# Performance work log

Measured on AMD Instinct MI355X. Metric: run time of the kernel, lower is better.

The kernel has to match this reference:

```python
import jax, jax.numpy as jnp
import numpy as np

B, T, C = 8, 1024, 1024
H, D = 16, 64  # num_heads, head_size

def setup_inputs() -> dict:
    key = jax.random.key(0)
    ks = jax.random.split(key, 6)
    s = C ** -0.5
    return {
        "x": jax.random.normal(ks[0], (B, T, C), dtype=jnp.float32),
        "Wq": jax.random.normal(ks[1], (H, C, D), dtype=jnp.float32) * s,
        "Wk": jax.random.normal(ks[2], (H, C, D), dtype=jnp.float32) * s,
        "Wv": jax.random.normal(ks[3], (H, C, D), dtype=jnp.float32) * s,
        "Wproj": jax.random.normal(ks[4], (H * D, C), dtype=jnp.float32) * ((H * D) ** -0.5),
        "bproj": jnp.zeros((C,), dtype=jnp.float32),
    }

def reference(x, Wq, Wk, Wv, Wproj, bproj):
    # per-head QKV projections, batched over heads via einsum (same math as looped heads)
    q = jnp.einsum('btc,hcd->bhtd', x, Wq)
    k = jnp.einsum('btc,hcd->bhtd', x, Wk)
    v = jnp.einsum('btc,hcd->bhtd', x, Wv)
    scale = D ** -0.5  # k.shape[-1]**-0.5 in original head
    scores = jnp.einsum('bhtd,bhsd->bhts', q, k) * scale  # [B,H,T,T]
    Tn = x.shape[1]
    causal = jnp.tril(jnp.ones((Tn, Tn), dtype=bool))
    scores = jnp.where(causal, scores, jnp.float32(-jnp.inf))
    att = jax.nn.softmax(scores, axis=-1)
    out = jnp.einsum('bhts,bhsd->bhtd', att, v)          # [B,H,T,D]
    out = out.transpose(0, 2, 1, 3).reshape(x.shape[0], Tn, H * D)  # concat heads
    return out @ Wproj + bproj  # dropout is identity at p=0.0
```

## Files before the change

### kernel.cpp

```cpp
#include <hip/hip_runtime.h>
#include <hip/hip_bf16.h>

#define B_ 8
#define T_ 1024
#define C_ 1024
#define H_ 16
#define D_ 64
#define QKVLD 3072

typedef short v8s __attribute__((ext_vector_type(8)));
typedef float v4f __attribute__((ext_vector_type(4)));
typedef float v16f __attribute__((ext_vector_type(16)));

__device__ __forceinline__ unsigned short f2b(float f) {
    unsigned int u = __builtin_bit_cast(unsigned int, f);
    unsigned int lsb = (u >> 16) & 1u;
    u += 0x7fffu + lsb;
    return (unsigned short)(u >> 16);
}

__device__ __forceinline__ float fexp2(float x) {
#if __has_builtin(__builtin_amdgcn_exp2f)
    return __builtin_amdgcn_exp2f(x);
#else
    return __expf(x * 0.69314718056f);
#endif
}

#define GLOAD16(gp, lp)                                                          \
    __builtin_amdgcn_global_load_lds(                                            \
        (const __attribute__((address_space(1))) unsigned int*)(gp),             \
        (__attribute__((address_space(3))) unsigned int*)(lp), 16, 0, 0)

__global__ void cast_x_kernel(const float* __restrict__ x, unsigned short* __restrict__ y, int n) {
    int i = (blockIdx.x * 256 + threadIdx.x) * 4;
    if (i < n) {
        float4 v = *(const float4*)(x + i);
        ushort4 o;
        o.x = f2b(v.x); o.y = f2b(v.y); o.z = f2b(v.z); o.w = f2b(v.w);
        *(ushort4*)(y + i) = o;
    }
}

__global__ void transpose_wqkv(const float* __restrict__ Wq, const float* __restrict__ Wk,
                               const float* __restrict__ Wv, unsigned short* __restrict__ WqkvT) {
    int z = blockIdx.y;
    int h = z / 3, part = z % 3;
    const float* src = (part == 0 ? Wq : (part == 1 ? Wk : Wv)) + (size_t)h * C_ * D_;
    int c0 = blockIdx.x * 64;
    __shared__ unsigned short t[64][65];
    for (int i = threadIdx.x; i < 4096; i += 256) {
        int r = i >> 6, d = i & 63;
        t[d][r] = f2b(src[(size_t)(c0 + r) * D_ + d]);
    }
    __syncthreads();
    unsigned short* dst = WqkvT + (size_t)(h * 192 + part * 64) * C_;
    for (int i = threadIdx.x; i < 4096; i += 256) {
        int d = i >> 6, r = i & 63;
        dst[(size_t)d * C_ + c0 + r] = t[d][r];
    }
}

__global__ void transpose_wproj(const float* __restrict__ W, unsigned short* __restrict__ Wt) {
    int k0 = blockIdx.y * 64, n0 = blockIdx.x * 64;
    __shared__ unsigned short t[64][65];
    for (int i = threadIdx.x; i < 4096; i += 256) {
        int r = i >> 6, c = i & 63;
        t[c][r] = f2b(W[(size_t)(k0 + r) * C_ + n0 + c]);
    }
    __syncthreads();
    for (int i = threadIdx.x; i < 4096; i += 256) {
        int n = i >> 6, k = i & 63;
        Wt[(size_t)(n0 + n) * 1024 + k0 + k] = t[n][k];
    }
}

template<int WRITE_MODE>
__global__ __launch_bounds__(256, 2) void gemm_bt(const unsigned short* __restrict__ A,
                                                  const unsigned short* __restrict__ Bt,
                                                  void* __restrict__ Cout,
                                                  const float* __restrict__ bias,
                                                  int M, int N, int K) {
    __shared__ unsigned short lA[2][256 * 32];
    __shared__ unsigned short lB[2][128 * 32];
    int tid = threadIdx.x;
    int m0 = blockIdx.y * 256, n0 = blockIdx.x * 128;
    int lane = tid & 63, w = tid >> 6;
    int half = lane >> 5, l32 = lane & 31;
    int wm = w >> 1, wn = w & 1;

    const unsigned short* gA[4];
    int offA[4];
    #pragma unroll
    for (int j = 0; j < 4; j++) {
        int c = j * 256 + tid;
        int row = c >> 2;
        int col8 = ((c & 3) ^ ((row >> 1) & 3)) * 8;
        gA[j] = A + (size_t)(m0 + row) * K + col8;
        offA[j] = (j * 256 + w * 64) * 16;
    }
    const unsigned short* gB[2];
    int offB[2];
    #pragma unroll
    for (int j = 0; j < 2; j++) {
        int c = j * 256 + tid;
        int row = c >> 2;
        int col8 = ((c & 3) ^ ((row >> 1) & 3)) * 8;
        gB[j] = Bt + (size_t)(n0 + row) * K + col8;
        offB[j] = (j * 256 + w * 64) * 16;
    }

    int am[4], bn[2];
    #pragma unroll
    for (int mi = 0; mi < 4; mi++) am[mi] = wm * 128 + mi * 32 + l32;
    #pragma unroll
    for (int ni = 0; ni < 2; ni++) bn[ni] = wn * 64 + ni * 32 + l32;

    v16f acc[4][2];
    #pragma unroll
    for (int mi = 0; mi < 4; mi++)
        #pragma unroll
        for (int ni = 0; ni < 2; ni++)
            #pragma unroll
            for (int r = 0; r < 16; r++) acc[mi][ni][r] = 0.f;

    int ktiles = K >> 5;
    #pragma unroll
    for (int j = 0; j < 4; j++) GLOAD16(gA[j], (char*)&lA[0][0] + offA[j]);
    #pragma unroll
    for (int j = 0; j < 2; j++) GLOAD16(gB[j], (char*)&lB[0][0] + offB[j]);

    for (int it = 0; it < ktiles; it++) {
        int cur = it & 1, nxt = cur ^ 1;
        __asm__ volatile("s_waitcnt vmcnt(0)" ::: "memory");
        __asm__ volatile("s_barrier" ::: "memory");
        {
            int kn = (it + 1 < ktiles) ? (it + 1) * 32 : it * 32;
            #pragma unroll
            for (int j = 0; j < 4; j++) GLOAD16(gA[j] + kn, (char*)&lA[nxt][0] + offA[j]);
            #pragma unroll
            for (int j = 0; j < 2; j++) GLOAD16(gB[j] + kn, (char*)&lB[nxt][0] + offB[j]);
        }
        #pragma unroll
        for (int step = 0; step < 2; step++) {
            int g = step * 2 + half;
            v8s af[4], bf[2];
            #pragma unroll
            for (int mi = 0; mi < 4; mi++)
                af[mi] = *(const v8s*)&lA[cur][am[mi] * 32 + ((g ^ ((am[mi] >> 1) & 3)) * 8)];
            #pragma unroll
            for (int ni = 0; ni < 2; ni++)
                bf[ni] = *(const v8s*)&lB[cur][bn[ni] * 32 + ((g ^ ((bn[ni] >> 1) & 3)) * 8)];
            #pragma unroll
            for (int mi = 0; mi < 4; mi++)
                #pragma unroll
                for (int ni = 0; ni < 2; ni++)
                    acc[mi][ni] = __builtin_amdgcn_mfma_f32_32x32x16_bf16(af[mi], bf[ni], acc[mi][ni], 0, 0, 0);
        }
    }
    #pragma unroll
    for (int mi = 0; mi < 4; mi++) {
        #pragma unroll
        for (int ni = 0; ni < 2; ni++) {
            int col = n0 + wn * 64 + ni * 32 + l32;
            #pragma unroll
            for (int r = 0; r < 16; r++) {
                int row = m0 + wm * 128 + mi * 32 + (r & 3) + 8 * (r >> 2) + 4 * half;
                float v = acc[mi][ni][r];
                if (WRITE_MODE == 1)
                    ((float*)Cout)[(size_t)row * N + col] = v + bias[col];
                else
                    ((unsigned short*)Cout)[(size_t)row * N + col] = f2b(v);
            }
        }
    }
}

__global__ void transpose_v(const unsigned short* __restrict__ QKV, unsigned short* __restrict__ Vt) {
    int t0 = blockIdx.x * 64;
    int bh = blockIdx.y;
    int b = bh >> 4, h = bh & 15;
    __shared__ unsigned short t[64][65];
    for (int i = threadIdx.x; i < 4096; i += 256) {
        int r = i >> 6, d = i & 63;
        t[d][r] = QKV[(size_t)(b * T_ + t0 + r) * QKVLD + h * 192 + 128 + d];
    }
    __syncthreads();
    for (int i = threadIdx.x; i < 4096; i += 256) {
        int d = i >> 6, r = i & 63;
        Vt[((size_t)bh * 64 + d) * T_ + t0 + r] = t[d][r];
    }
}

__global__ __launch_bounds__(256) void attn_kernel(const unsigned short* __restrict__ QKV,
                                                   const unsigned short* __restrict__ Vt,
                                                   unsigned short* __restrict__ Ob) {
    int bh = blockIdx.x;
    int qt = 7 - blockIdx.y;
    int b = bh >> 4, h = bh & 15;
    int tid = threadIdx.x, lane = tid & 63, w = tid >> 6;
    int quad = lane >> 4, l16 = lane & 15;
    int qg0 = qt * 128 + w * 32;

    __shared__ unsigned short lK[2][2][64][32];
    __shared__ unsigned short lV[2][64][32];
    __shared__ unsigned short lP[4][32][76];

    v8s aq[2][2];
    #pragma unroll
    for (int st = 0; st < 2; st++) {
        const unsigned short* qp = QKV + (size_t)(b * T_ + qg0 + st * 16 + l16) * QKVLD + h * 192;
        aq[st][0] = *(const v8s*)(qp + quad * 8);
        aq[st][1] = *(const v8s*)(qp + 32 + quad * 8);
    }

    const unsigned short* gK[2];
    const unsigned short* gV[2];
    int ldsOff[2];
    #pragma unroll
    for (int j = 0; j < 2; j++) {
        int c = j * 256 + tid;
        int halfp = c >> 8, row = (c >> 2) & 63;
        int col8 = ((c & 3) ^ ((row >> 1) & 3)) * 8;
        gK[j] = QKV + (size_t)(b * T_ + row) * QKVLD + h * 192 + 64 + halfp * 32 + col8;
        gV[j] = Vt + ((size_t)bh * 64 + row) * T_ + halfp * 32 + col8;
        ldsOff[j] = (j * 256 + w * 64) * 16;
    }
    int rcol = (quad ^ ((l16 >> 1) & 3)) * 8;

    v4f accO[2][4];
    float lsum[2][4];
    #pragma unroll
    for (int st = 0; st < 2; st++)
        #pragma unroll
        for (int i = 0; i < 4; i++) { accO[st][i] = (v4f){0.f, 0.f, 0.f, 0.f}; lsum[st][i] = 0.f; }

    int ntiles = 2 * qt + 2;
    const float SC = 0.1803368801f;

    #pragma unroll
    for (int j = 0; j < 2; j++)
        GLOAD16(gK[j], (char*)&lK[0][0][0][0] + ldsOff[j]);

    for (int it = 0; it < ntiles; it++) {
        int cur = it & 1, nxt = cur ^ 1;
        int s0 = it * 64;
        __asm__ volatile("s_waitcnt vmcnt(0)" ::: "memory");
        __asm__ volatile("s_barrier" ::: "memory");
        #pragma unroll
        for (int j = 0; j < 2; j++)
            GLOAD16(gV[j] + s0, (char*)&lV[0][0][0] + ldsOff[j]);
        __asm__ volatile("" ::: "memory");
        {
            int itn = (it + 1 < ntiles) ? it + 1 : it;
            size_t koff = (size_t)itn * 64 * QKVLD;
            #pragma unroll
            for (int j = 0; j < 2; j++)
                GLOAD16(gK[j] + koff, (char*)&lK[nxt][0][0][0] + ldsOff[j]);
        }
        bool act0 = (qg0 + 15 >= s0);
        bool act1 = (qg0 + 31 >= s0);
        if (act1) {
            v4f sf[2][4];
            #pragma unroll
            for (int nt = 0; nt < 4; nt++) {
                v8s bk0 = *(const v8s*)&lK[cur][0][nt * 16 + l16][rcol];
                v8s bk1 = *(const v8s*)&lK[cur][1][nt * 16 + l16][rcol];
                if (act0) {
                    v4f a = (v4f){0.f, 0.f, 0.f, 0.f};
                    a = __builtin_amdgcn_mfma_f32_16x16x32_bf16(aq[0][0], bk0, a, 0, 0, 0);
                    a = __builtin_amdgcn_mfma_f32_16x16x32_bf16(aq[0][1], bk1, a, 0, 0, 0);
                    sf[0][nt] = a;
                }
                v4f a1 = (v4f){0.f, 0.f, 0.f, 0.f};
                a1 = __builtin_amdgcn_mfma_f32_16x16x32_bf16(aq[1][0], bk0, a1, 0, 0, 0);
                a1 = __builtin_amdgcn_mfma_f32_16x16x32_bf16(aq[1][1], bk1, a1, 0, 0, 0);
                sf[1][nt] = a1;
            }
            bool diag = (it >= ntiles - 2);
            #pragma unroll
            for (int st = 0; st < 2; st++) {
                if (st == 0 && !act0) continue;
                if (diag) {
                    #pragma unroll
                    for (int nt = 0; nt < 4; nt++)
                        #pragma unroll
                        for (int r = 0; r < 4; r++) {
                            int sg = s0 + nt * 16 + l16;
                            int qg = qg0 + st * 16 + quad * 4 + r;
                            float p = (sg > qg) ? 0.f : fexp2(sf[st][nt][r] * SC);
                            lsum[st][r] += p;
                            lP[w][st * 16 + quad * 4 + r][nt * 16 + l16] = f2b(p);
                        }
                } else {
                    #pragma unroll
                    for (int nt = 0; nt < 4; nt++)
                        #pragma unroll
                        for (int r = 0; r < 4; r++) {
                            float p = fexp2(sf[st][nt][r] * SC);
                            lsum[st][r] += p;
                            lP[w][st * 16 + quad * 4 + r][nt * 16 + l16] = f2b(p);
                        }
                }
            }
        }
        __asm__ volatile("s_waitcnt vmcnt(2)" ::: "memory");
        __asm__ volatile("s_barrier" ::: "memory");
        __asm__ volatile("s_waitcnt lgkmcnt(0)" ::: "memory");
        if (act1) {
            #pragma unroll
            for (int sc = 0; sc < 2; sc++) {
                v8s ap0, ap1;
                if (act0) ap0 = *(const v8s*)&lP[w][l16][sc * 32 + quad * 8];
                ap1 = *(const v8s*)&lP[w][16 + l16][sc * 32 + quad * 8];
                #pragma unroll
                for (int dt = 0; dt < 4; dt++) {
                    v8s bv = *(const v8s*)&lV[sc][dt * 16 + l16][rcol];
                    if (act0) accO[0][dt] = __builtin_amdgcn_mfma_f32_16x16x32_bf16(ap0, bv, accO[0][dt], 0, 0, 0);
                    accO[1][dt] = __builtin_amdgcn_mfma_f32_16x16x32_bf16(ap1, bv, accO[1][dt], 0, 0, 0);
                }
            }
        }
    }
    #pragma unroll
    for (int st = 0; st < 2; st++)
        #pragma unroll
        for (int r = 0; r < 4; r++) {
            float s = lsum[st][r];
            #pragma unroll
            for (int off = 1; off < 16; off <<= 1) s += __shfl_xor(s, off, 64);
            float inv = 1.0f / s;
            int q = qg0 + st * 16 + quad * 4 + r;
            #pragma unroll
            for (int dt = 0; dt < 4; dt++) {
                int d = dt * 16 + l16;
                Ob[(size_t)(b * T_ + q) * (H_ * D_) + h * 64 + d] = f2b(accO[st][dt][r] * inv);
            }
        }
}

extern "C" void kernel_launch(void* const* d_in, const int* in_sizes, int n_in,
                              void* d_out, int out_size, void* d_ws, size_t ws_size,
                              hipStream_t stream) {
    const float* x     = (const float*)d_in[0];
    const float* Wq    = (const float*)d_in[1];
    const float* Wk    = (const float*)d_in[2];
    const float* Wv    = (const float*)d_in[3];
    const float* Wproj = (const float*)d_in[4];
    const float* bproj = (const float*)d_in[5];
    float* out = (float*)d_out;

    char* ws = (char*)d_ws;
    unsigned short* xb     = (unsigned short*)ws;
    unsigned short* WqkvT  = (unsigned short*)(ws + 16777216);
    unsigned short* WprojT = (unsigned short*)(ws + 23068672);
    unsigned short* QKV    = (unsigned short*)(ws + 25165824);
    unsigned short* Vt     = (unsigned short*)(ws + 75497472);
    unsigned short* Ob     = (unsigned short*)(ws + 92274688);

    cast_x_kernel<<<dim3(8192), dim3(256), 0, stream>>>(x, xb, B_ * T_ * C_);
    transpose_wqkv<<<dim3(16, 48), dim3(256), 0, stream>>>(Wq, Wk, Wv, WqkvT);
    transpose_wproj<<<dim3(16, 16), dim3(256), 0, stream>>>(Wproj, WprojT);
    gemm_bt<0><<<dim3(24, 32), dim3(256), 0, stream>>>(xb, WqkvT, QKV, nullptr, 8192, 3072, 1024);
    transpose_v<<<dim3(16, 128), dim3(256), 0, stream>>>(QKV, Vt);
    attn_kernel<<<dim3(128, 8), dim3(256), 0, stream>>>(QKV, Vt, Ob);
    gemm_bt<1><<<dim3(8, 32), dim3(256), 0, stream>>>(Ob, WprojT, out, bproj, 8192, 1024, 1024);
}
```

Measured before the change: 266.0 us.

## Triple-buffer GEMM loads, remap blocks per XCD, shrink output-projection tile

The bf16 GEMM moves from double to triple buffering in LDS with a partial vmcnt wait, so two k-tiles of global loads stay in flight while the current tile is computed. Block indices are linearized and remapped so each XCD handles a contiguous stripe of M rows, aiming at better L2 reuse of A. The output projection switches to a 128-row tile with more blocks and higher occupancy to fill the GPU better. The cost is more LDS per block and more complex indexing, and the 4-way tile now needs 72KB of LDS, which may limit residency.

Result: no change. 262.3 us (-1.4%).

```diff
diff --git a/kernel.cpp b/kernel.cpp
--- a/kernel.cpp
+++ b/kernel.cpp
@@ -75,24 +75,35 @@
     }
 }
 
-template<int WRITE_MODE>
-__global__ __launch_bounds__(256, 2) void gemm_bt(const unsigned short* __restrict__ A,
-                                                  const unsigned short* __restrict__ Bt,
-                                                  void* __restrict__ Cout,
-                                                  const float* __restrict__ bias,
-                                                  int M, int N, int K) {
-    __shared__ unsigned short lA[2][256 * 32];
-    __shared__ unsigned short lB[2][128 * 32];
+template<int MB, int WRITE_MODE>
+__global__ __launch_bounds__(256, (MB == 4) ? 2 : 3)
+void gemm_bt(const unsigned short* __restrict__ A,
+             const unsigned short* __restrict__ Bt,
+             void* __restrict__ Cout,
+             const float* __restrict__ bias,
+             int M, int N, int K) {
+    constexpr int BM = MB * 64;
+    constexpr int ABUF = BM * 32;
+    constexpr int BBUF = 128 * 32;
+    __shared__ unsigned short lA[3 * ABUF];
+    __shared__ unsigned short lB[3 * BBUF];
+
     int tid = threadIdx.x;
-    int m0 = blockIdx.y * 256, n0 = blockIdx.x * 128;
     int lane = tid & 63, w = tid >> 6;
     int half = lane >> 5, l32 = lane & 31;
     int wm = w >> 1, wn = w & 1;
 
-    const unsigned short* gA[4];
-    int offA[4];
-    #pragma unroll
-    for (int j = 0; j < 4; j++) {
+    int g = blockIdx.x;
+    int nbm = M / BM;
+    int stripe = nbm >> 3;
+    int xcd = g & 7, s = g >> 3;
+    int m0 = (xcd * stripe + (s % stripe)) * BM;
+    int n0 = (s / stripe) * 128;
+
+    const unsigned short* gA[MB];
+    int offA[MB];
+    #pragma unroll
+    for (int j = 0; j < MB; j++) {
         int c = j * 256 + tid;
         int row = c >> 2;
         int col8 = ((c & 3) ^ ((row >> 1) & 3)) * 8;
@@ -110,62 +121,71 @@
         offB[j] = (j * 256 + w * 64) * 16;
     }
 
-    int am[4], bn[2];
-    #pragma unroll
-    for (int mi = 0; mi < 4; mi++) am[mi] = wm * 128 + mi * 32 + l32;
+    int am[MB], bn[2];
+    #pragma unroll
+    for (int mi = 0; mi < MB; mi++) am[mi] = wm * (MB * 32) + mi * 32 + l32;
     #pragma unroll
     for (int ni = 0; ni < 2; ni++) bn[ni] = wn * 64 + ni * 32 + l32;
 
-    v16f acc[4][2];
-    #pragma unroll
-    for (int mi = 0; mi < 4; mi++)
+    v16f acc[MB][2];
+    #pragma unroll
+    for (int mi = 0; mi < MB; mi++)
         #pragma unroll
         for (int ni = 0; ni < 2; ni++)
             #pragma unroll
             for (int r = 0; r < 16; r++) acc[mi][ni][r] = 0.f;
 
-    int ktiles = K >> 5;
-    #pragma unroll
-    for (int j = 0; j < 4; j++) GLOAD16(gA[j], (char*)&lA[0][0] + offA[j]);
-    #pragma unroll
-    for (int j = 0; j < 2; j++) GLOAD16(gB[j], (char*)&lB[0][0] + offB[j]);
-
-    for (int it = 0; it < ktiles; it++) {
-        int cur = it & 1, nxt = cur ^ 1;
-        __asm__ volatile("s_waitcnt vmcnt(0)" ::: "memory");
+    int kt = K >> 5;
+    #pragma unroll
+    for (int j = 0; j < MB; j++) GLOAD16(gA[j], (char*)lA + offA[j]);
+    #pragma unroll
+    for (int j = 0; j < 2; j++) GLOAD16(gB[j], (char*)lB + offB[j]);
+    #pragma unroll
+    for (int j = 0; j < MB; j++) GLOAD16(gA[j] + 32, (char*)(lA + ABUF) + offA[j]);
+    #pragma unroll
+    for (int j = 0; j < 2; j++) GLOAD16(gB[j] + 32, (char*)(lB + BBUF) + offB[j]);
+
+    int cur = 0;
+    for (int it = 0; it < kt; it++) {
+        int nx2 = cur + 2; if (nx2 >= 3) nx2 -= 3;
+        if constexpr (MB == 4) __asm__ volatile("s_waitcnt vmcnt(6)" ::: "memory");
+        else                   __asm__ volatile("s_waitcnt vmcnt(4)" ::: "memory");
         __asm__ volatile("s_barrier" ::: "memory");
         {
-            int kn = (it + 1 < ktiles) ? (it + 1) * 32 : it * 32;
-            #pragma unroll
-            for (int j = 0; j < 4; j++) GLOAD16(gA[j] + kn, (char*)&lA[nxt][0] + offA[j]);
-            #pragma unroll
-            for (int j = 0; j < 2; j++) GLOAD16(gB[j] + kn, (char*)&lB[nxt][0] + offB[j]);
-        }
+            int kn = ((it + 2 < kt) ? it + 2 : kt - 1) << 5;
+            #pragma unroll
+            for (int j = 0; j < MB; j++) GLOAD16(gA[j] + kn, (char*)(lA + nx2 * ABUF) + offA[j]);
+            #pragma unroll
+            for (int j = 0; j < 2; j++) GLOAD16(gB[j] + kn, (char*)(lB + nx2 * BBUF) + offB[j]);
+        }
+        const unsigned short* bufA = lA + cur * ABUF;
+        const unsigned short* bufB = lB + cur * BBUF;
         #pragma unroll
         for (int step = 0; step < 2; step++) {
-            int g = step * 2 + half;
-            v8s af[4], bf[2];
-            #pragma unroll
-            for (int mi = 0; mi < 4; mi++)
-                af[mi] = *(const v8s*)&lA[cur][am[mi] * 32 + ((g ^ ((am[mi] >> 1) & 3)) * 8)];
+            int gch = step * 2 + half;
+            v8s af[MB], bf[2];
+            #pragma unroll
+            for (int mi = 0; mi < MB; mi++)
+                af[mi] = *(const v8s*)&bufA[am[mi] * 32 + ((gch ^ ((am[mi] >> 1) & 3)) * 8)];
             #pragma unroll
             for (int ni = 0; ni < 2; ni++)
-                bf[ni] = *(const v8s*)&lB[cur][bn[ni] * 32 + ((g ^ ((bn[ni] >> 1) & 3)) * 8)];
-            #pragma unroll
-            for (int mi = 0; mi < 4; mi++)
+                bf[ni] = *(const v8s*)&bufB[bn[ni] * 32 + ((gch ^ ((bn[ni] >> 1) & 3)) * 8)];
+            #pragma unroll
+            for (int mi = 0; mi < MB; mi++)
                 #pragma unroll
                 for (int ni = 0; ni < 2; ni++)
                     acc[mi][ni] = __builtin_amdgcn_mfma_f32_32x32x16_bf16(af[mi], bf[ni], acc[mi][ni], 0, 0, 0);
         }
-    }
-    #pragma unroll
-    for (int mi = 0; mi < 4; mi++) {
+        cur = cur + 1; if (cur >= 3) cur -= 3;
+    }
+    #pragma unroll
+    for (int mi = 0; mi < MB; mi++) {
         #pragma unroll
         for (int ni = 0; ni < 2; ni++) {
             int col = n0 + wn * 64 + ni * 32 + l32;
             #pragma unroll
             for (int r = 0; r < 16; r++) {
-                int row = m0 + wm * 128 + mi * 32 + (r & 3) + 8 * (r >> 2) + 4 * half;
+                int row = m0 + wm * (MB * 32) + mi * 32 + (r & 3) + 8 * (r >> 2) + 4 * half;
                 float v = acc[mi][ni][r];
                 if (WRITE_MODE == 1)
                     ((float*)Cout)[(size_t)row * N + col] = v + bias[col];
@@ -361,8 +381,8 @@
     cast_x_kernel<<<dim3(8192), dim3(256), 0, stream>>>(x, xb, B_ * T_ * C_);
     transpose_wqkv<<<dim3(16, 48), dim3(256), 0, stream>>>(Wq, Wk, Wv, WqkvT);
     transpose_wproj<<<dim3(16, 16), dim3(256), 0, stream>>>(Wproj, WprojT);
-    gemm_bt<0><<<dim3(24, 32), dim3(256), 0, stream>>>(xb, WqkvT, QKV, nullptr, 8192, 3072, 1024);
+    gemm_bt<4, 0><<<dim3(768), dim3(256), 0, stream>>>(xb, WqkvT, QKV, nullptr, 8192, 3072, 1024);
     transpose_v<<<dim3(16, 128), dim3(256), 0, stream>>>(QKV, Vt);
     attn_kernel<<<dim3(128, 8), dim3(256), 0, stream>>>(QKV, Vt, Ob);
-    gemm_bt<1><<<dim3(8, 32), dim3(256), 0, stream>>>(Ob, WprojT, out, bproj, 8192, 1024, 1024);
-}
+    gemm_bt<2, 1><<<dim3(512), dim3(256), 0, stream>>>(Ob, WprojT, out, bproj, 8192, 1024, 1024);
+}
```

## Specialize output projection GEMM with 128x128 tiles, triple buffering, XCD-aware block mapping

Applied to the files above, without the earlier changes.

Splits the templated GEMM into a QKV variant and a dedicated projection kernel. The projection GEMM switches to 128x128 tiles, giving 512 blocks instead of 256 so the CUs are better filled. It also adds a three-stage LDS pipeline with two loads in flight and remaps block IDs so each XCD handles a contiguous stripe of M rows, improving L2 reuse of A. The smaller tiles lower MFMA reuse per LDS load.

Result: faster. 241.9 us (-9.1%).

```diff
diff --git a/kernel.cpp b/kernel.cpp
--- a/kernel.cpp
+++ b/kernel.cpp
@@ -75,12 +75,10 @@
     }
 }
 
-template<int WRITE_MODE>
-__global__ __launch_bounds__(256, 2) void gemm_bt(const unsigned short* __restrict__ A,
-                                                  const unsigned short* __restrict__ Bt,
-                                                  void* __restrict__ Cout,
-                                                  const float* __restrict__ bias,
-                                                  int M, int N, int K) {
+__global__ __launch_bounds__(256, 2) void gemm_qkv(const unsigned short* __restrict__ A,
+                                                   const unsigned short* __restrict__ Bt,
+                                                   unsigned short* __restrict__ Cout,
+                                                   int M, int N, int K) {
     __shared__ unsigned short lA[2][256 * 32];
     __shared__ unsigned short lB[2][128 * 32];
     int tid = threadIdx.x;
@@ -166,11 +164,120 @@
             #pragma unroll
             for (int r = 0; r < 16; r++) {
                 int row = m0 + wm * 128 + mi * 32 + (r & 3) + 8 * (r >> 2) + 4 * half;
-                float v = acc[mi][ni][r];
-                if (WRITE_MODE == 1)
-                    ((float*)Cout)[(size_t)row * N + col] = v + bias[col];
-                else
-                    ((unsigned short*)Cout)[(size_t)row * N + col] = f2b(v);
+                Cout[(size_t)row * N + col] = f2b(acc[mi][ni][r]);
+            }
+        }
+    }
+}
+
+__global__ __launch_bounds__(256, 3) void gemm_proj(const unsigned short* __restrict__ A,
+                                                    const unsigned short* __restrict__ Bt,
+                                                    float* __restrict__ Cout,
+                                                    const float* __restrict__ bias,
+                                                    int M, int N, int K) {
+    constexpr int ABUF = 128 * 32;
+    constexpr int BBUF = 128 * 32;
+    __shared__ unsigned short lA[3 * ABUF];
+    __shared__ unsigned short lB[3 * BBUF];
+
+    int tid = threadIdx.x;
+    int lane = tid & 63, w = tid >> 6;
+    int half = lane >> 5, l32 = lane & 31;
+    int wm = w >> 1, wn = w & 1;
+
+    int g = blockIdx.x;
+    int nbm = M / 128;
+    int stripe = nbm >> 3;
+    int xcd = g & 7, s = g >> 3;
+    int m0 = (xcd * stripe + (s % stripe)) * 128;
+    int n0 = (s / stripe) * 128;
+
+    const unsigned short* gA[2];
+    int offA[2];
+    #pragma unroll
+    for (int j = 0; j < 2; j++) {
+        int c = j * 256 + tid;
+        int row = c >> 2;
+        int col8 = ((c & 3) ^ ((row >> 1) & 3)) * 8;
+        gA[j] = A + (size_t)(m0 + row) * K + col8;
+        offA[j] = (j * 256 + w * 64) * 16;
+    }
+    const unsigned short* gB[2];
+    int offB[2];
+    #pragma unroll
+    for (int j = 0; j < 2; j++) {
+        int c = j * 256 + tid;
+        int row = c >> 2;
+        int col8 = ((c & 3) ^ ((row >> 1) & 3)) * 8;
+        gB[j] = Bt + (size_t)(n0 + row) * K + col8;
+        offB[j] = (j * 256 + w * 64) * 16;
+    }
+
+    int am[2], bn[2];
+    #pragma unroll
+    for (int mi = 0; mi < 2; mi++) am[mi] = wm * 64 + mi * 32 + l32;
+    #pragma unroll
+    for (int ni = 0; ni < 2; ni++) bn[ni] = wn * 64 + ni * 32 + l32;
+
+    v16f acc[2][2];
+    #pragma unroll
+    for (int mi = 0; mi < 2; mi++)
+        #pragma unroll
+        for (int ni = 0; ni < 2; ni++)
+            #pragma unroll
+            for (int r = 0; r < 16; r++) acc[mi][ni][r] = 0.f;
+
+    int kt = K >> 5;
+    #pragma unroll
+    for (int j = 0; j < 2; j++) GLOAD16(gA[j], (char*)lA + offA[j]);
+    #pragma unroll
+    for (int j = 0; j < 2; j++) GLOAD16(gB[j], (char*)lB + offB[j]);
+    #pragma unroll
+    for (int j = 0; j < 2; j++) GLOAD16(gA[j] + 32, (char*)(lA + ABUF) + offA[j]);
+    #pragma unroll
+    for (int j = 0; j < 2; j++) GLOAD16(gB[j] + 32, (char*)(lB + BBUF) + offB[j]);
+
+    int cur = 0;
+    for (int it = 0; it < kt; it++) {
+        int nx2 = cur + 2; if (nx2 >= 3) nx2 -= 3;
+        __asm__ volatile("s_waitcnt vmcnt(4)" ::: "memory");
+        __asm__ volatile("s_barrier" ::: "memory");
+        {
+            int kn = ((it + 2 < kt) ? it + 2 : kt - 1) << 5;
+            #pragma unroll
+            for (int j = 0; j < 2; j++) GLOAD16(gA[j] + kn, (char*)(lA + nx2 * ABUF) + offA[j]);
+            #pragma unroll
+            for (int j = 0; j < 2; j++) GLOAD16(gB[j] + kn, (char*)(lB + nx2 * BBUF) + offB[j]);
+        }
+        const unsigned short* bufA = lA + cur * ABUF;
+        const unsigned short* bufB = lB + cur * BBUF;
+        #pragma unroll
+        for (int step = 0; step < 2; step++) {
+            int gch = step * 2 + half;
+            v8s af[2], bf[2];
+            #pragma unroll
+            for (int mi = 0; mi < 2; mi++)
+                af[mi] = *(const v8s*)&bufA[am[mi] * 32 + ((gch ^ ((am[mi] >> 1) & 3)) * 8)];
+            #pragma unroll
+            for (int ni = 0; ni < 2; ni++)
+                bf[ni] = *(const v8s*)&bufB[bn[ni] * 32 + ((gch ^ ((bn[ni] >> 1) & 3)) * 8)];
+            #pragma unroll
+            for (int mi = 0; mi < 2; mi++)
+                #pragma unroll
+                for (int ni = 0; ni < 2; ni++)
+                    acc[mi][ni] = __builtin_amdgcn_mfma_f32_32x32x16_bf16(af[mi], bf[ni], acc[mi][ni], 0, 0, 0);
+        }
+        cur = cur + 1; if (cur >= 3) cur -= 3;
+    }
+    #pragma unroll
+    for (int mi = 0; mi < 2; mi++) {
+        #pragma unroll
+        for (int ni = 0; ni < 2; ni++) {
+            int col = n0 + wn * 64 + ni * 32 + l32;
+            #pragma unroll
+            for (int r = 0; r < 16; r++) {
+                int row = m0 + wm * 64 + mi * 32 + (r & 3) + 8 * (r >> 2) + 4 * half;
+                Cout[(size_t)row * N + col] = acc[mi][ni][r] + bias[col];
             }
         }
     }
@@ -361,8 +468,8 @@
     cast_x_kernel<<<dim3(8192), dim3(256), 0, stream>>>(x, xb, B_ * T_ * C_);
     transpose_wqkv<<<dim3(16, 48), dim3(256), 0, stream>>>(Wq, Wk, Wv, WqkvT);
     transpose_wproj<<<dim3(16, 16), dim3(256), 0, stream>>>(Wproj, WprojT);
-    gemm_bt<0><<<dim3(24, 32), dim3(256), 0, stream>>>(xb, WqkvT, QKV, nullptr, 8192, 3072, 1024);
+    gemm_qkv<<<dim3(24, 32), dim3(256), 0, stream>>>(xb, WqkvT, QKV, 8192, 3072, 1024);
     transpose_v<<<dim3(16, 128), dim3(256), 0, stream>>>(QKV, Vt);
     attn_kernel<<<dim3(128, 8), dim3(256), 0, stream>>>(QKV, Vt, Ob);
-    gemm_bt<1><<<dim3(8, 32), dim3(256), 0, stream>>>(Ob, WprojT, out, bproj, 8192, 1024, 1024);
-}
+    gemm_proj<<<dim3(512), dim3(256), 0, stream>>>(Ob, WprojT, out, bproj, 8192, 1024, 1024);
+}
```
